# Performance work log

Measured on AMD Instinct MI355X. Metric: run time of the kernel, lower is better.

## Reference

```python
import jax, jax.numpy as jnp
import numpy as np

V, E, H, B, S = 32000, 1024, 1024, 64, 128


def setup_inputs() -> dict:
    key = jax.random.key(0)
    ks = jax.random.split(key, 16)
    s = 0.02
    return {
        "input_seq": jax.random.randint(ks[0], (B, 1), 0, V),
        "hidden": jax.random.normal(ks[1], (1, B, H), jnp.float32),
        "cell": jax.random.normal(ks[2], (1, B, H), jnp.float32),
        "encoder_outputs": jax.random.normal(ks[3], (B, S, H), jnp.float32),
        "emb": jax.random.normal(ks[4], (V, E), jnp.float32) * s,
        "Wa_w": jax.random.normal(ks[5], (H, H), jnp.float32) * s,
        "Wa_b": jnp.zeros((H,), jnp.float32),
        "Ua_w": jax.random.normal(ks[6], (H, H), jnp.float32) * s,
        "Ua_b": jnp.zeros((H,), jnp.float32),
        "Va_w": jax.random.normal(ks[7], (1, H), jnp.float32) * s,
        "Va_b": jnp.zeros((1,), jnp.float32),
        "W_ih": jax.random.normal(ks[8], (4 * H, E + H), jnp.float32) * s,
        "W_hh": jax.random.normal(ks[9], (4 * H, H), jnp.float32) * s,
        "b_ih": jnp.zeros((4 * H,), jnp.float32),
        "b_hh": jnp.zeros((4 * H,), jnp.float32),
        "out_w": jax.random.normal(ks[10], (V, H), jnp.float32) * s,
        "out_b": jnp.zeros((V,), jnp.float32),
    }


def reference(input_seq, hidden, cell, encoder_outputs, emb, Wa_w, Wa_b, Ua_w, Ua_b,
              Va_w, Va_b, W_ih, W_hh, b_ih, b_hh, out_w, out_b):
    # embedding lookup (dropout p=0 -> identity): [B,1,E]
    embedded = emb[input_seq]
    # query = last layer hidden: [B,1,H]
    query = hidden[-1][:, None, :]
    # Bahdanau additive attention
    q_proj = query @ Wa_w.T + Wa_b                       # [B,1,H]
    k_proj = encoder_outputs @ Ua_w.T + Ua_b             # [B,S,H]
    scores = jnp.tanh(q_proj + k_proj) @ Va_w.T + Va_b   # [B,S,1]
    scores = scores[..., 0][:, None, :]                  # [B,1,S]
    weights = jax.nn.softmax(scores, axis=-1)            # [B,1,S]
    context = jnp.einsum('bqs,bsh->bqh', weights, encoder_outputs)  # [B,1,H]
    # LSTM single step on concat(embedded, context)
    x = jnp.concatenate([embedded, context], axis=2)[:, 0, :]  # [B,E+H]
    h0, c0 = hidden[0], cell[0]
    gates = x @ W_ih.T + b_ih + h0 @ W_hh.T + b_hh       # [B,4H]
    i, f, g, o = jnp.split(gates, 4, axis=-1)
    c1 = jax.nn.sigmoid(f) * c0 + jax.nn.sigmoid(i) * jnp.tanh(g)
    h1 = jax.nn.sigmoid(o) * jnp.tanh(c1)
    output = h1[:, None, :]                              # [B,1,H]
    logits = output @ out_w.T + out_b                    # [B,1,V]
    return logits, h1[None], c1[None], weights
```

## Files before the change

### kernel.cpp

```cpp
#include <hip/hip_runtime.h>
#include <hip/hip_bf16.h>

using short8 = __attribute__((ext_vector_type(8))) short;
using f32x4  = __attribute__((ext_vector_type(4))) float;

__device__ inline unsigned pk2(float lo, float hi) {
    __hip_bfloat162 h = __float22bfloat162_rn(float2{lo, hi});
    return *reinterpret_cast<unsigned*>(&h);
}
__device__ inline short8 cvt8(float4 a, float4 b) {
    union { unsigned u[4]; short8 s; } r;
    r.u[0] = pk2(a.x, a.y); r.u[1] = pk2(a.z, a.w);
    r.u[2] = pk2(b.x, b.y); r.u[3] = pk2(b.z, b.w);
    return r.s;
}
__device__ inline float ftanh(float x) {
    float e = __expf(2.f * x);
    return 1.f - 2.f / (e + 1.f);
}
__device__ inline void gload16(const void* g, void* lds) {
    __builtin_amdgcn_global_load_lds(
        (const __attribute__((address_space(1))) unsigned int*)g,
        (__attribute__((address_space(3))) unsigned int*)lds, 16, 0, 0);
}
__device__ inline short f2b(float f) {
    unsigned u = __float_as_uint(f);
    return (short)((u + 0x7FFFu + ((u >> 16) & 1u)) >> 16);
}

__global__ void k_init(const int* __restrict__ idx, const float* __restrict__ emb,
                       const float* __restrict__ h0, float* __restrict__ xcat,
                       float4* __restrict__ wsz) {
    int i = blockIdx.x * blockDim.x + threadIdx.x;
    if (i < 18432) {
        float4 z = {0.f, 0.f, 0.f, 0.f};
        wsz[i] = z;
    } else if (i < 67584) {
        int j = i - 18432;
        int b = j / 768, q = j - b * 768;
        if (q < 256)
            ((float4*)(xcat + (size_t)b * 3072))[q] =
                ((const float4*)(emb + (size_t)idx[b] * 1024))[q];
        else if (q >= 512)
            ((float4*)(xcat + (size_t)b * 3072))[q] =
                ((const float4*)(h0 + (size_t)b * 1024))[q - 512];
    }
}

__global__ void k_cvt_swz(const float* __restrict__ enc, const float* __restrict__ Ua,
                          short* __restrict__ dst) {
    int i = blockIdx.x * blockDim.x + threadIdx.x;
    if (i >= 9216 * 128) return;
    int row = i >> 7, gi = i & 127;
    int seg = gi >> 3, g = gi & 7;
    const float* src = (row < 8192) ? enc + ((size_t)row << 10)
                                    : Ua + ((size_t)(row - 8192) << 10);
    const float* p = src + (seg << 6) + ((g ^ (row & 7)) << 3);
    float4 v0 = *(const float4*)p;
    float4 v1 = *(const float4*)(p + 4);
    *(short8*)&dst[(size_t)i << 3] = cvt8(v0, v1);
}

__global__ __launch_bounds__(512) void k_attn2(
    const short* __restrict__ Abf, const short* __restrict__ Bbf,
    const float* __restrict__ Uab, const float* __restrict__ Wab,
    const float* __restrict__ qp, const float* __restrict__ Va,
    float* __restrict__ scores) {
    __shared__ short As[256 * 64];
    __shared__ short Bs[128 * 64];
    const int t = threadIdx.x;
    const int l = t & 63, w = t >> 6;
    const int wm = w >> 1, wn = w & 1;
    const int lr = l & 15, lg = l >> 4;
    const int n0 = blockIdx.x * 128;
    const int r0 = blockIdx.y * 256;

    f32x4 acc[4][4];
#pragma unroll
    for (int i = 0; i < 4; ++i)
#pragma unroll
        for (int j = 0; j < 4; ++j) { f32x4 z = {0.f, 0.f, 0.f, 0.f}; acc[i][j] = z; }

    for (int seg = 0; seg < 16; ++seg) {
#pragma unroll
        for (int i = 0; i < 4; ++i) {
            int base = i * 512 + w * 64;
            int s = base + l;
            gload16(Abf + (((size_t)r0 + (s >> 3)) << 10) + (seg << 6) + ((s & 7) << 3),
                    (void*)&As[base * 8]);
            if (i < 2)
                gload16(Bbf + (((size_t)8192 + n0 + (s >> 3)) << 10) + (seg << 6) + ((s & 7) << 3),
                        (void*)&Bs[base * 8]);
        }
        __syncthreads();
#pragma unroll
        for (int kh = 0; kh < 2; ++kh) {
            short8 a[4], b[4];
#pragma unroll
            for (int i = 0; i < 4; ++i) {
                int ra = wm * 64 + i * 16 + lr;
                a[i] = *(const short8*)&As[ra * 64 + (((kh * 4 + lg) ^ (ra & 7)) << 3)];
                int rb = wn * 64 + i * 16 + lr;
                b[i] = *(const short8*)&Bs[rb * 64 + (((kh * 4 + lg) ^ (rb & 7)) << 3)];
            }
#pragma unroll
            for (int i = 0; i < 4; ++i)
#pragma unroll
                for (int j = 0; j < 4; ++j)
                    acc[i][j] = __builtin_amdgcn_mfma_f32_16x16x32_bf16(a[i], b[j], acc[i][j], 0, 0, 0);
        }
        __syncthreads();
    }

    float va[4], ub[4];
#pragma unroll
    for (int j = 0; j < 4; ++j) {
        int h = n0 + wn * 64 + j * 16 + lr;
        va[j] = Va[h];
        ub[j] = Uab[h] + Wab[h];
    }
#pragma unroll
    for (int i = 0; i < 4; ++i)
#pragma unroll
        for (int r = 0; r < 4; ++r) {
            int row = r0 + wm * 64 + i * 16 + lg * 4 + r;
            const float* qpb = qp + (size_t)(row >> 7) * 1024;
            float s = 0.f;
#pragma unroll
            for (int j = 0; j < 4; ++j) {
                int h = n0 + wn * 64 + j * 16 + lr;
                s += va[j] * ftanh(acc[i][j][r] + qpb[h] + ub[j]);
            }
            s += __shfl_xor(s, 1);
            s += __shfl_xor(s, 2);
            s += __shfl_xor(s, 4);
            s += __shfl_xor(s, 8);
            if (lr == 0) atomicAdd(scores + row, s);
        }
}

template <int EPI>
__global__ __launch_bounds__(256) void k_sgemm(
    const float* __restrict__ A, int lda,
    const float* __restrict__ B0, int ldb0,
    const float* __restrict__ B1, int ldb1, int kyB1,
    float* __restrict__ C, int ldc, int Kblk, int pstride) {
    __shared__ short As[64 * 64];
    __shared__ short Bs[64 * 64];
    const int t = threadIdx.x;
    const int l = t & 63, w = t >> 6;
    const int wm = w >> 1, wn = w & 1;
    const int lr = l & 15, lg = l >> 4;
    const int n0 = blockIdx.x * 64;
    const int ky = blockIdx.y;

    const float* Ab = A + (size_t)ky * Kblk;
    const float* Bb;
    int ldb;
    if (ky < kyB1) { Bb = B0 + (size_t)ky * Kblk; ldb = ldb0; }
    else           { Bb = B1 + (size_t)(ky - kyB1) * Kblk; ldb = ldb1; }

    f32x4 acc[2][2];
#pragma unroll
    for (int i = 0; i < 2; ++i)
#pragma unroll
        for (int j = 0; j < 2; ++j) { f32x4 z = {0.f, 0.f, 0.f, 0.f}; acc[i][j] = z; }

    for (int kt = 0; kt < Kblk; kt += 64) {
#pragma unroll
        for (int i = 0; i < 2; ++i) {
            int s = t + 256 * i, row = s >> 3, ch = s & 7;
            const float* p = Ab + (size_t)row * lda + kt + ch * 8;
            *(short8*)&As[row * 64 + ((ch ^ (row & 7)) << 3)] =
                cvt8(*(const float4*)p, *(const float4*)(p + 4));
            const float* q = Bb + (size_t)(n0 + row) * ldb + kt + ch * 8;
            *(short8*)&Bs[row * 64 + ((ch ^ (row & 7)) << 3)] =
                cvt8(*(const float4*)q, *(const float4*)(q + 4));
        }
        __syncthreads();
#pragma unroll
        for (int kh = 0; kh < 2; ++kh) {
            short8 a[2], b[2];
#pragma unroll
            for (int i = 0; i < 2; ++i) {
                int ra = wm * 32 + i * 16 + lr;
                a[i] = *(const short8*)&As[ra * 64 + (((kh * 4 + lg) ^ (ra & 7)) << 3)];
                int rb = wn * 32 + i * 16 + lr;
                b[i] = *(const short8*)&Bs[rb * 64 + (((kh * 4 + lg) ^ (rb & 7)) << 3)];
            }
#pragma unroll
            for (int i = 0; i < 2; ++i)
#pragma unroll
                for (int j = 0; j < 2; ++j)
                    acc[i][j] = __builtin_amdgcn_mfma_f32_16x16x32_bf16(a[i], b[j], acc[i][j], 0, 0, 0);
        }
        __syncthreads();
    }

    float* Cp = (EPI == 0) ? C + (size_t)ky * pstride : C;
#pragma unroll
    for (int i = 0; i < 2; ++i)
#pragma unroll
        for (int j = 0; j < 2; ++j)
#pragma unroll
            for (int r = 0; r < 4; ++r) {
                int R = wm * 32 + i * 16 + lg * 4 + r;
                int c = n0 + wn * 32 + j * 16 + lr;
                if constexpr (EPI == 1)
                    atomicAdd(&C[(size_t)R * ldc + c], acc[i][j][r]);
                else
                    Cp[(size_t)R * ldc + c] = acc[i][j][r];
            }
}

__global__ __launch_bounds__(256) void k_vgemm(
    const short* __restrict__ Abf,
    const float* __restrict__ B,
    const float* __restrict__ bias,
    float* __restrict__ C) {
    const int t = threadIdx.x;
    const int l = t & 63, w = t >> 6;
    const int lr = l & 15, lg = l >> 4;
    const int n0 = blockIdx.x * 64 + w * 16;

    f32x4 acc[4];
#pragma unroll
    for (int i = 0; i < 4; ++i) { f32x4 z = {0.f, 0.f, 0.f, 0.f}; acc[i] = z; }

    const float* bp = B + (size_t)(n0 + lr) * 1024 + lg * 8;
    const short* ap = Abf + lr * 1024 + lg * 8;

#pragma unroll 4
    for (int k0 = 0; k0 < 1024; k0 += 32) {
        float4 b0 = *(const float4*)(bp + k0);
        float4 b1 = *(const float4*)(bp + k0 + 4);
        short8 a0 = *(const short8*)(ap + k0);
        short8 a1 = *(const short8*)(ap + k0 + 16 * 1024);
        short8 a2 = *(const short8*)(ap + k0 + 32 * 1024);
        short8 a3 = *(const short8*)(ap + k0 + 48 * 1024);
        short8 bf = cvt8(b0, b1);
        acc[0] = __builtin_amdgcn_mfma_f32_16x16x32_bf16(a0, bf, acc[0], 0, 0, 0);
        acc[1] = __builtin_amdgcn_mfma_f32_16x16x32_bf16(a1, bf, acc[1], 0, 0, 0);
        acc[2] = __builtin_amdgcn_mfma_f32_16x16x32_bf16(a2, bf, acc[2], 0, 0, 0);
        acc[3] = __builtin_amdgcn_mfma_f32_16x16x32_bf16(a3, bf, acc[3], 0, 0, 0);
    }

    float bv = bias[n0 + lr];
#pragma unroll
    for (int i = 0; i < 4; ++i)
#pragma unroll
        for (int r = 0; r < 4; ++r)
            C[(size_t)(i * 16 + lg * 4 + r) * 32000 + n0 + lr] = acc[i][r] + bv;
}

__global__ __launch_bounds__(256) void k_smctx(
    const float* __restrict__ scores, const float* __restrict__ enc,
    float* __restrict__ wout, float* __restrict__ xcat) {
    int b = blockIdx.x;
    int t = threadIdx.x;
    __shared__ float buf[128];
    __shared__ float wsb[128];
    if (t < 128) buf[t] = scores[b * 128 + t];
    __syncthreads();
    if (t < 64) buf[t] = fmaxf(buf[t], buf[t + 64]);
    __syncthreads();
    if (t < 32) buf[t] = fmaxf(buf[t], buf[t + 32]);
    __syncthreads();
    float m;
    {
        float v = buf[t & 31];
        for (int off = 16; off > 0; off >>= 1)
            v = fmaxf(v, __shfl_xor(v, off, 32));
        m = v;
    }
    __syncthreads();
    if (t < 128) wsb[t] = __expf(scores[b * 128 + t] - m);
    __syncthreads();
    if (t < 64) buf[t] = wsb[t] + wsb[t + 64];
    __syncthreads();
    if (t < 32) buf[t] += buf[t + 32];
    __syncthreads();
    float sum;
    {
        float v = buf[t & 31];
        for (int off = 16; off > 0; off >>= 1)
            v += __shfl_xor(v, off, 32);
        sum = v;
    }
    float inv = 1.f / sum;
    __syncthreads();
    if (t < 128) {
        wsb[t] *= inv;
        wout[b * 128 + t] = wsb[t];
    }
    __syncthreads();
    float acc[4] = {0.f, 0.f, 0.f, 0.f};
    for (int s = 0; s < 128; ++s) {
        float wv = wsb[s];
        const float* row = enc + ((size_t)b * 128 + s) * 1024;
#pragma unroll
        for (int j = 0; j < 4; ++j) acc[j] += wv * row[t + 256 * j];
    }
#pragma unroll
    for (int j = 0; j < 4; ++j) xcat[(size_t)b * 3072 + 1024 + t + 256 * j] = acc[j];
}

__global__ void k_lstm6(const float* __restrict__ gp, const float* __restrict__ c0,
                        const float* __restrict__ b_ih, const float* __restrict__ b_hh,
                        float* __restrict__ h1, float* __restrict__ c1,
                        short* __restrict__ h1bf) {
    int idx = blockIdx.x * blockDim.x + threadIdx.x;
    int b = idx >> 10, h = idx & 1023;
    const float* g0 = gp + (size_t)b * 4096;
    float iv = b_ih[h] + b_hh[h];
    float fv = b_ih[1024 + h] + b_hh[1024 + h];
    float gv = b_ih[2048 + h] + b_hh[2048 + h];
    float ov = b_ih[3072 + h] + b_hh[3072 + h];
#pragma unroll
    for (int p = 0; p < 6; ++p) {
        const float* g = g0 + p * 262144;
        iv += g[h];
        fv += g[1024 + h];
        gv += g[2048 + h];
        ov += g[3072 + h];
    }
    float si = 1.f / (1.f + expf(-iv));
    float sf = 1.f / (1.f + expf(-fv));
    float so = 1.f / (1.f + expf(-ov));
    float tg = tanhf(gv);
    float cc = sf * c0[idx] + si * tg;
    float hh = so * tanhf(cc);
    c1[idx] = cc;
    h1[idx] = hh;
    h1bf[idx] = f2b(hh);
}

extern "C" void kernel_launch(void* const* d_in, const int* in_sizes, int n_in,
                              void* d_out, int out_size, void* d_ws, size_t ws_size,
                              hipStream_t stream) {
    const int* idx = (const int*)d_in[0];
    const float* hidden = (const float*)d_in[1];
    const float* cell = (const float*)d_in[2];
    const float* enc = (const float*)d_in[3];
    const float* emb = (const float*)d_in[4];
    const float* Wa_w = (const float*)d_in[5];
    const float* Wa_b = (const float*)d_in[6];
    const float* Ua_w = (const float*)d_in[7];
    const float* Ua_b = (const float*)d_in[8];
    const float* Va_w = (const float*)d_in[9];
    const float* W_ih = (const float*)d_in[11];
    const float* W_hh = (const float*)d_in[12];
    const float* b_ih = (const float*)d_in[13];
    const float* b_hh = (const float*)d_in[14];
    const float* out_w = (const float*)d_in[15];
    const float* out_b = (const float*)d_in[16];

    float* out = (float*)d_out;
    float* logits = out;
    float* h1 = out + 2048000;
    float* c1 = out + 2048000 + 65536;
    float* wts = out + 2048000 + 65536 + 65536;

    float* ws = (float*)d_ws;
    float* qp = ws;
    float* scores = ws + 65536;
    float* xcat = ws + 73728;
    float* gates_p = ws + 270336;
    short* h1_bf = (short*)(ws + 1843200);
    short* encua_bf = (short*)(ws + 1908736);

    k_init<<<264, 256, 0, stream>>>(idx, emb, hidden, xcat, (float4*)ws);
    k_cvt_swz<<<4608, 256, 0, stream>>>(enc, Ua_w, encua_bf);
    k_sgemm<1><<<dim3(16, 8), 256, 0, stream>>>(hidden, 1024, Wa_w, 1024,
                                                nullptr, 0, 99, qp, 1024, 128, 0);
    k_attn2<<<dim3(8, 32), 512, 0, stream>>>(encua_bf, encua_bf, Ua_b, Wa_b,
                                             qp, Va_w, scores);
    k_smctx<<<64, 256, 0, stream>>>(scores, enc, wts, xcat);
    k_sgemm<0><<<dim3(64, 6), 256, 0, stream>>>(xcat, 3072, W_ih, 2048,
                                                W_hh, 1024, 4, gates_p, 4096, 512, 262144);
    k_lstm6<<<256, 256, 0, stream>>>(gates_p, cell, b_ih, b_hh, h1, c1, h1_bf);
    k_vgemm<<<500, 256, 0, stream>>>(h1_bf, out_w, out_b, logits);
}
```

Baseline: 137.0 us.

## Stream gate weights with single-wave MFMA kernel using bf16 activations

Stores the concatenated LSTM input (embedding, context, h0) as bf16 instead of fp32. The gates GEMM now uses a new streaming kernel with one wave per 16 output columns, split three ways over K, in place of the LDS-tiled sgemm with six K-splits. This cuts the partial-sum traffic in the LSTM kernel from six passes to three. The logits GEMM is also recast from 256-thread blocks to 64-thread blocks (2000 blocks), which spreads the weight stream over more, smaller blocks at the cost of more launch-level scheduling work.

```diff
diff --git a/kernel.cpp b/kernel.cpp
--- a/kernel.cpp
+++ b/kernel.cpp
@@ -29,21 +29,24 @@
 }
 
 __global__ void k_init(const int* __restrict__ idx, const float* __restrict__ emb,
-                       const float* __restrict__ h0, float* __restrict__ xcat,
+                       const float* __restrict__ h0, short* __restrict__ xcat_bf,
                        float4* __restrict__ wsz) {
     int i = blockIdx.x * blockDim.x + threadIdx.x;
     if (i < 18432) {
         float4 z = {0.f, 0.f, 0.f, 0.f};
         wsz[i] = z;
-    } else if (i < 67584) {
+    } else if (i < 34816) {
         int j = i - 18432;
-        int b = j / 768, q = j - b * 768;
-        if (q < 256)
-            ((float4*)(xcat + (size_t)b * 3072))[q] =
-                ((const float4*)(emb + (size_t)idx[b] * 1024))[q];
-        else if (q >= 512)
-            ((float4*)(xcat + (size_t)b * 3072))[q] =
-                ((const float4*)(h0 + (size_t)b * 1024))[q - 512];
+        int b = j >> 8, g = j & 255;
+        if (g < 128) {
+            const float* p = emb + (size_t)idx[b] * 1024 + g * 8;
+            *(short8*)&xcat_bf[b * 3072 + g * 8] =
+                cvt8(*(const float4*)p, *(const float4*)(p + 4));
+        } else {
+            const float* p = h0 + (size_t)b * 1024 + (g - 128) * 8;
+            *(short8*)&xcat_bf[b * 3072 + 2048 + (g - 128) * 8] =
+                cvt8(*(const float4*)p, *(const float4*)(p + 4));
+        }
     }
 }
 
@@ -139,12 +142,10 @@
         }
 }
 
-template <int EPI>
 __global__ __launch_bounds__(256) void k_sgemm(
     const float* __restrict__ A, int lda,
     const float* __restrict__ B0, int ldb0,
-    const float* __restrict__ B1, int ldb1, int kyB1,
-    float* __restrict__ C, int ldc, int Kblk, int pstride) {
+    float* __restrict__ C, int ldc, int Kblk) {
     __shared__ short As[64 * 64];
     __shared__ short Bs[64 * 64];
     const int t = threadIdx.x;
@@ -155,10 +156,7 @@
     const int ky = blockIdx.y;
 
     const float* Ab = A + (size_t)ky * Kblk;
-    const float* Bb;
-    int ldb;
-    if (ky < kyB1) { Bb = B0 + (size_t)ky * Kblk; ldb = ldb0; }
-    else           { Bb = B1 + (size_t)(ky - kyB1) * Kblk; ldb = ldb1; }
+    const float* Bb = B0 + (size_t)ky * Kblk;
 
     f32x4 acc[2][2];
 #pragma unroll
@@ -173,7 +171,7 @@
             const float* p = Ab + (size_t)row * lda + kt + ch * 8;
             *(short8*)&As[row * 64 + ((ch ^ (row & 7)) << 3)] =
                 cvt8(*(const float4*)p, *(const float4*)(p + 4));
-            const float* q = Bb + (size_t)(n0 + row) * ldb + kt + ch * 8;
+            const float* q = Bb + (size_t)(n0 + row) * ldb0 + kt + ch * 8;
             *(short8*)&Bs[row * 64 + ((ch ^ (row & 7)) << 3)] =
                 cvt8(*(const float4*)q, *(const float4*)(q + 4));
         }
@@ -197,7 +195,6 @@
         __syncthreads();
     }
 
-    float* Cp = (EPI == 0) ? C + (size_t)ky * pstride : C;
 #pragma unroll
     for (int i = 0; i < 2; ++i)
 #pragma unroll
@@ -206,39 +203,73 @@
             for (int r = 0; r < 4; ++r) {
                 int R = wm * 32 + i * 16 + lg * 4 + r;
                 int c = n0 + wn * 32 + j * 16 + lr;
-                if constexpr (EPI == 1)
-                    atomicAdd(&C[(size_t)R * ldc + c], acc[i][j][r]);
-                else
-                    Cp[(size_t)R * ldc + c] = acc[i][j][r];
+                atomicAdd(&C[(size_t)R * ldc + c], acc[i][j][r]);
             }
 }
 
-__global__ __launch_bounds__(256) void k_vgemm(
-    const short* __restrict__ Abf,
-    const float* __restrict__ B,
-    const float* __restrict__ bias,
-    float* __restrict__ C) {
-    const int t = threadIdx.x;
-    const int l = t & 63, w = t >> 6;
+__global__ __launch_bounds__(64) void k_gates_s(
+    const short* __restrict__ Abf, const float* __restrict__ Wih,
+    const float* __restrict__ Whh, float* __restrict__ gp) {
+    const int l = threadIdx.x;
     const int lr = l & 15, lg = l >> 4;
-    const int n0 = blockIdx.x * 64 + w * 16;
+    const int n0 = blockIdx.x * 16;
+    const int ky = blockIdx.y;
+    const float* Bb = (ky == 0) ? Wih : (ky == 1) ? Wih + 1024 : Whh;
+    const int ldb = (ky < 2) ? 2048 : 1024;
 
     f32x4 acc[4];
 #pragma unroll
     for (int i = 0; i < 4; ++i) { f32x4 z = {0.f, 0.f, 0.f, 0.f}; acc[i] = z; }
 
-    const float* bp = B + (size_t)(n0 + lr) * 1024 + lg * 8;
-    const short* ap = Abf + lr * 1024 + lg * 8;
+    const short* ap = Abf + lr * 3072 + ky * 1024 + lg * 8;
+    const float* bp = Bb + (size_t)(n0 + lr) * ldb + lg * 8;
 
 #pragma unroll 4
     for (int k0 = 0; k0 < 1024; k0 += 32) {
         float4 b0 = *(const float4*)(bp + k0);
         float4 b1 = *(const float4*)(bp + k0 + 4);
+        short8 bf = cvt8(b0, b1);
+        short8 a0 = *(const short8*)(ap + k0);
+        short8 a1 = *(const short8*)(ap + k0 + 16 * 3072);
+        short8 a2 = *(const short8*)(ap + k0 + 32 * 3072);
+        short8 a3 = *(const short8*)(ap + k0 + 48 * 3072);
+        acc[0] = __builtin_amdgcn_mfma_f32_16x16x32_bf16(a0, bf, acc[0], 0, 0, 0);
+        acc[1] = __builtin_amdgcn_mfma_f32_16x16x32_bf16(a1, bf, acc[1], 0, 0, 0);
+        acc[2] = __builtin_amdgcn_mfma_f32_16x16x32_bf16(a2, bf, acc[2], 0, 0, 0);
+        acc[3] = __builtin_amdgcn_mfma_f32_16x16x32_bf16(a3, bf, acc[3], 0, 0, 0);
+    }
+
+    float* Cp = gp + (size_t)ky * 262144;
+#pragma unroll
+    for (int i = 0; i < 4; ++i)
+#pragma unroll
+        for (int r = 0; r < 4; ++r)
+            Cp[(size_t)(i * 16 + lg * 4 + r) * 4096 + n0 + lr] = acc[i][r];
+}
+
+__global__ __launch_bounds__(64) void k_logits_s(
+    const short* __restrict__ Abf, const float* __restrict__ B,
+    const float* __restrict__ bias, float* __restrict__ C) {
+    const int l = threadIdx.x;
+    const int lr = l & 15, lg = l >> 4;
+    const int n0 = blockIdx.x * 16;
+
+    f32x4 acc[4];
+#pragma unroll
+    for (int i = 0; i < 4; ++i) { f32x4 z = {0.f, 0.f, 0.f, 0.f}; acc[i] = z; }
+
+    const short* ap = Abf + lr * 1024 + lg * 8;
+    const float* bp = B + (size_t)(n0 + lr) * 1024 + lg * 8;
+
+#pragma unroll 4
+    for (int k0 = 0; k0 < 1024; k0 += 32) {
+        float4 b0 = *(const float4*)(bp + k0);
+        float4 b1 = *(const float4*)(bp + k0 + 4);
+        short8 bf = cvt8(b0, b1);
         short8 a0 = *(const short8*)(ap + k0);
         short8 a1 = *(const short8*)(ap + k0 + 16 * 1024);
         short8 a2 = *(const short8*)(ap + k0 + 32 * 1024);
         short8 a3 = *(const short8*)(ap + k0 + 48 * 1024);
-        short8 bf = cvt8(b0, b1);
         acc[0] = __builtin_amdgcn_mfma_f32_16x16x32_bf16(a0, bf, acc[0], 0, 0, 0);
         acc[1] = __builtin_amdgcn_mfma_f32_16x16x32_bf16(a1, bf, acc[1], 0, 0, 0);
         acc[2] = __builtin_amdgcn_mfma_f32_16x16x32_bf16(a2, bf, acc[2], 0, 0, 0);
@@ -255,7 +286,7 @@
 
 __global__ __launch_bounds__(256) void k_smctx(
     const float* __restrict__ scores, const float* __restrict__ enc,
-    float* __restrict__ wout, float* __restrict__ xcat) {
+    float* __restrict__ wout, short* __restrict__ xcat_bf) {
     int b = blockIdx.x;
     int t = threadIdx.x;
     __shared__ float buf[128];
@@ -302,10 +333,11 @@
         for (int j = 0; j < 4; ++j) acc[j] += wv * row[t + 256 * j];
     }
 #pragma unroll
-    for (int j = 0; j < 4; ++j) xcat[(size_t)b * 3072 + 1024 + t + 256 * j] = acc[j];
-}
-
-__global__ void k_lstm6(const float* __restrict__ gp, const float* __restrict__ c0,
+    for (int j = 0; j < 4; ++j)
+        xcat_bf[(size_t)b * 3072 + 1024 + t + 256 * j] = f2b(acc[j]);
+}
+
+__global__ void k_lstm3(const float* __restrict__ gp, const float* __restrict__ c0,
                         const float* __restrict__ b_ih, const float* __restrict__ b_hh,
                         float* __restrict__ h1, float* __restrict__ c1,
                         short* __restrict__ h1bf) {
@@ -317,7 +349,7 @@
     float gv = b_ih[2048 + h] + b_hh[2048 + h];
     float ov = b_ih[3072 + h] + b_hh[3072 + h];
 #pragma unroll
-    for (int p = 0; p < 6; ++p) {
+    for (int p = 0; p < 3; ++p) {
         const float* g = g0 + p * 262144;
         iv += g[h];
         fv += g[1024 + h];
@@ -364,20 +396,19 @@
     float* ws = (float*)d_ws;
     float* qp = ws;
     float* scores = ws + 65536;
-    float* xcat = ws + 73728;
-    float* gates_p = ws + 270336;
-    short* h1_bf = (short*)(ws + 1843200);
-    short* encua_bf = (short*)(ws + 1908736);
-
-    k_init<<<264, 256, 0, stream>>>(idx, emb, hidden, xcat, (float4*)ws);
+    short* xcat_bf = (short*)(ws + 73728);
+    float* gates_p = ws + 172032;
+    short* h1_bf = (short*)(ws + 958464);
+    short* encua_bf = (short*)(ws + 991232);
+
+    k_init<<<136, 256, 0, stream>>>(idx, emb, hidden, xcat_bf, (float4*)ws);
     k_cvt_swz<<<4608, 256, 0, stream>>>(enc, Ua_w, encua_bf);
-    k_sgemm<1><<<dim3(16, 8), 256, 0, stream>>>(hidden, 1024, Wa_w, 1024,
-                                                nullptr, 0, 99, qp, 1024, 128, 0);
+    k_sgemm<<<dim3(16, 8), 256, 0, stream>>>(hidden, 1024, Wa_w, 1024,
+                                             qp, 1024, 128);
     k_attn2<<<dim3(8, 32), 512, 0, stream>>>(encua_bf, encua_bf, Ua_b, Wa_b,
                                              qp, Va_w, scores);
-    k_smctx<<<64, 256, 0, stream>>>(scores, enc, wts, xcat);
-    k_sgemm<0><<<dim3(64, 6), 256, 0, stream>>>(xcat, 3072, W_ih, 2048,
-                                                W_hh, 1024, 4, gates_p, 4096, 512, 262144);
-    k_lstm6<<<256, 256, 0, stream>>>(gates_p, cell, b_ih, b_hh, h1, c1, h1_bf);
-    k_vgemm<<<500, 256, 0, stream>>>(h1_bf, out_w, out_b, logits);
-}
+    k_smctx<<<64, 256, 0, stream>>>(scores, enc, wts, xcat_bf);
+    k_gates_s<<<dim3(256, 3), 64, 0, stream>>>(xcat_bf, W_ih, W_hh, gates_p);
+    k_lstm3<<<256, 256, 0, stream>>>(gates_p, cell, b_ih, b_hh, h1, c1, h1_bf);
+    k_logits_s<<<2000, 64, 0, stream>>>(h1_bf, out_w, out_b, logits);
+}
```

New measurement: 140.5 us. +2.6%, slower.
